# Kernel optimization log

Measured on AMD Instinct MI355X. Metric: run time of the kernel, lower is better.

## Reference

```python
import jax, jax.numpy as jnp
import numpy as np

B, T, C, H = 2, 4096, 1024, 16
HD = C // H  # head dim = 64


def setup_inputs() -> dict:
    key = jax.random.key(0)
    ks = jax.random.split(key, 5)
    s = 1.0 / np.sqrt(C)
    return {
        "x": jax.random.normal(ks[0], (B, T, C), jnp.float32),
        # stored as (in, out) so forward is x @ w + b (equiv to torch Linear with W^T)
        "w_attn": jax.random.normal(ks[1], (C, 3 * C), jnp.float32) * s,
        "b_attn": jax.random.normal(ks[2], (3 * C,), jnp.float32) * 0.02,
        "w_proj": jax.random.normal(ks[3], (C, C), jnp.float32) * s,
        "b_proj": jax.random.normal(ks[4], (C,), jnp.float32) * 0.02,
    }


def reference(x, w_attn, b_attn, w_proj, b_proj):
    # qkv projection: (B,T,3C) -> split into q,k,v
    qkv = x @ w_attn + b_attn
    q, k, v = jnp.split(qkv, 3, axis=-1)
    # (B,T,C) -> (B,H,T,HD)
    def to_heads(t):
        return t.reshape(B, T, H, HD).transpose(0, 2, 1, 3)
    q, k, v = to_heads(q), to_heads(k), to_heads(v)
    # naive attention: explicit (B,H,T,T) scores, causal mask, softmax
    att = jnp.einsum("bhqd,bhkd->bhqk", q, k) * (1.0 / np.sqrt(HD))
    causal = jnp.tril(jnp.ones((T, T), bool))  # (T,T)
    att = jnp.where(causal[None, None], att, -jnp.inf)
    att = jax.nn.softmax(att, axis=-1)
    y = jnp.einsum("bhqk,bhkd->bhqd", att, v)  # (B,H,T,HD)
    y = y.transpose(0, 2, 1, 3).reshape(B, T, C)
    y = y @ w_proj + b_proj
    return (y, (k, v))
```

## Files before the change

kernel.cpp:

```cpp
#include <hip/hip_runtime.h>
#include <hip/hip_bf16.h>

typedef unsigned short u16;
typedef __attribute__((ext_vector_type(8))) short short8;
typedef __attribute__((ext_vector_type(4))) short s16x4;
typedef __attribute__((ext_vector_type(4))) float f32x4;

#define T_SEQ  4096
#define HEADS  16
#define HDIM   64
#define CDIM   1024
#define MDIM   8192
#define HSZ    (T_SEQ * HDIM)
#define SEC    8388608
#define QSCALE 0.1803368801111244f

__device__ __forceinline__ u16 f2bf(float f) {
    __hip_bfloat16 h = __float2bfloat16(f);
    u16 u; __builtin_memcpy(&u, &h, 2);
    return u;
}

__global__ __launch_bounds__(256) void cast_k(const float* __restrict__ in,
                                              u16* __restrict__ out, int n4) {
    const int i = blockIdx.x * 256 + threadIdx.x;
    if (i < n4) {
        f32x4 v = ((const f32x4*)in)[i];
        s16x4 o;
        #pragma unroll
        for (int j = 0; j < 4; ++j) o[j] = (short)f2bf(v[j]);
        ((s16x4*)out)[i] = o;
    }
}

template <int IN_F32>
__global__ __launch_bounds__(256) void transpose_k(const void* __restrict__ in_,
                                                   u16* __restrict__ out,
                                                   int R, int C) {
    __shared__ u16 tile[32][33];
    const size_t zoff = (size_t)blockIdx.z * R * C;
    const int c0 = blockIdx.x * 32, r0 = blockIdx.y * 32;
    const int tx = threadIdx.x, ty = threadIdx.y;
    #pragma unroll
    for (int i = ty; i < 32; i += 8) {
        const size_t idx = zoff + (size_t)(r0 + i) * C + c0 + tx;
        tile[i][tx] = IN_F32 ? f2bf(((const float*)in_)[idx])
                             : ((const u16*)in_)[idx];
    }
    __syncthreads();
    #pragma unroll
    for (int i = ty; i < 32; i += 8)
        out[zoff + (size_t)(c0 + i) * R + r0 + tx] = tile[tx][i];
}

template <int MODE>
__global__ __launch_bounds__(256) void gemm_k(const u16* __restrict__ A,
                                              const u16* __restrict__ Bt,
                                              const float* __restrict__ bias,
                                              float* __restrict__ outp,
                                              u16* __restrict__ qws,
                                              u16* __restrict__ kbf, int K) {
    __shared__ unsigned char sA[16384];
    __shared__ unsigned char sB[16384];
    const int tid  = threadIdx.x;
    const int lane = tid & 63;
    const int w = tid >> 6, wr = w >> 1, wc = w & 1;
    const int m0 = blockIdx.y * 128, n0 = blockIdx.x * 128;
    const int fr = lane & 15, fg = lane >> 4;

    f32x4 acc[4][4] = {};

    const int srow  = tid >> 1;
    const int scolb = (tid & 1) * 64;
    const u16* ga = A  + (size_t)(m0 + srow) * K + (tid & 1) * 32;
    const u16* gb = Bt + (size_t)(n0 + srow) * K + (tid & 1) * 32;
    unsigned char* wAr = sA + srow * 128;
    unsigned char* wBr = sB + srow * 128;
    const int swz  = (srow & 7) << 4;
    const int rswz = (fr & 7) << 4;

    const int nk = K >> 6;
    for (int kt = 0; kt < nk; ++kt) {
        short8 va0 = *(const short8*)(ga + 0);
        short8 va1 = *(const short8*)(ga + 8);
        short8 va2 = *(const short8*)(ga + 16);
        short8 va3 = *(const short8*)(ga + 24);
        short8 vb0 = *(const short8*)(gb + 0);
        short8 vb1 = *(const short8*)(gb + 8);
        short8 vb2 = *(const short8*)(gb + 16);
        short8 vb3 = *(const short8*)(gb + 24);
        ga += 64; gb += 64;
        __syncthreads();
        *(short8*)(wAr + ((scolb +  0) ^ swz)) = va0;
        *(short8*)(wAr + ((scolb + 16) ^ swz)) = va1;
        *(short8*)(wAr + ((scolb + 32) ^ swz)) = va2;
        *(short8*)(wAr + ((scolb + 48) ^ swz)) = va3;
        *(short8*)(wBr + ((scolb +  0) ^ swz)) = vb0;
        *(short8*)(wBr + ((scolb + 16) ^ swz)) = vb1;
        *(short8*)(wBr + ((scolb + 32) ^ swz)) = vb2;
        *(short8*)(wBr + ((scolb + 48) ^ swz)) = vb3;
        __syncthreads();
        #pragma unroll
        for (int kk = 0; kk < 2; ++kk) {
            short8 af[4], bf[4];
            #pragma unroll
            for (int m = 0; m < 4; ++m)
                af[m] = *(const short8*)(sA + (wr*64 + m*16 + fr) * 128 +
                                         ((kk*64 + fg*16) ^ rswz));
            #pragma unroll
            for (int n = 0; n < 4; ++n)
                bf[n] = *(const short8*)(sB + (wc*64 + n*16 + fr) * 128 +
                                         ((kk*64 + fg*16) ^ rswz));
            #pragma unroll
            for (int m = 0; m < 4; ++m)
                #pragma unroll
                for (int n = 0; n < 4; ++n)
                    acc[m][n] = __builtin_amdgcn_mfma_f32_16x16x32_bf16(
                        af[m], bf[n], acc[m][n], 0, 0, 0);
        }
    }

    #pragma unroll
    for (int n = 0; n < 4; ++n) {
        const int gn = n0 + wc*64 + n*16 + fr;
        const float bn = bias[gn];
        if (MODE == 0) {
            const int s = gn >> 10;
            const int c = gn & 1023;
            const int h = c >> 6, d = c & 63;
            if (s == 0) {
                #pragma unroll
                for (int m = 0; m < 4; ++m)
                    #pragma unroll
                    for (int r = 0; r < 4; ++r) {
                        const int gm = m0 + wr*64 + m*16 + fg*4 + r;
                        const int b = gm >> 12, t = gm & 4095;
                        qws[(size_t)((b << 4) + h) * HSZ + (size_t)t * HDIM + d] =
                            f2bf((acc[m][n][r] + bn) * QSCALE);
                    }
            } else {
                float* fdst = outp + (size_t)s * SEC;
                #pragma unroll
                for (int m = 0; m < 4; ++m)
                    #pragma unroll
                    for (int r = 0; r < 4; ++r) {
                        const int gm = m0 + wr*64 + m*16 + fg*4 + r;
                        const int b = gm >> 12, t = gm & 4095;
                        const size_t hidx =
                            (size_t)((b << 4) + h) * HSZ + (size_t)t * HDIM + d;
                        const float v = acc[m][n][r] + bn;
                        fdst[hidx] = v;
                        if (s == 1 && kbf) kbf[hidx] = f2bf(v);
                    }
            }
        } else {
            #pragma unroll
            for (int m = 0; m < 4; ++m)
                #pragma unroll
                for (int r = 0; r < 4; ++r) {
                    const int gm = m0 + wr*64 + m*16 + fg*4 + r;
                    outp[(size_t)gm * CDIM + gn] = acc[m][n][r] + bn;
                }
        }
    }
}

template <int KBF>
__global__ __launch_bounds__(256) void attn_k(const u16* __restrict__ q,
                                              const float* __restrict__ kf32,
                                              const u16* __restrict__ kb16,
                                              const u16* __restrict__ vt,
                                              u16* __restrict__ att) {
    __shared__ unsigned char sK[4096];
    __shared__ unsigned char sV[4096];
    __shared__ unsigned char sP[4096];
    const int wg  = blockIdx.x;
    const int xcd = wg & 7;
    const int i   = wg >> 3;
    const int bh  = xcd * 4 + (i >> 5);
    const int pair = i & 31;
    const int tid = threadIdx.x, lane = tid & 63, w = tid >> 6;
    const int fr = lane & 15, fg = lane >> 4;
    const size_t hbase = (size_t)bh * HSZ;

    const int krow = tid >> 3, kcolb = (tid & 7) * 16;
    const int swzK = (krow & 7) << 4;
    const int vrow = tid >> 2, vcolb = (tid & 3) * 16;
    const int swzV = (vrow & 3) << 4;
    const int rswzK = (fr & 7) << 4;
    const int rswzV = (fr & 3) << 4;
    const int rswzP = (((fr & 3) ^ ((fr >> 2) & 3)) << 4);

    const float* gkf = kf32 ? kf32 + hbase + (size_t)krow * 64 + (tid & 7) * 8 : nullptr;
    const u16*   gkb = kb16 ? kb16 + hbase + (size_t)krow * 64 + (tid & 7) * 8 : nullptr;
    const u16*   gv  = vt + hbase + (size_t)vrow * T_SEQ + (tid & 3) * 8;
    const int b = bh >> 4, h = bh & 15;

    #pragma unroll
    for (int ph = 0; ph < 2; ++ph) {
        const int qblk = ph ? 63 - pair : pair;
        const int q0 = qblk * 64 + w * 16;

        const short8 qf0 = *(const short8*)(q + hbase + (size_t)(q0 + fr) * 64 + fg * 8);
        const short8 qf1 = *(const short8*)(q + hbase + (size_t)(q0 + fr) * 64 + 32 + fg * 8);

        f32x4 o[4] = {};
        float srow[4] = {0.f, 0.f, 0.f, 0.f};

        const int nkt = 2 * (qblk + 1);
        for (int kt = 0; kt < nkt; ++kt) {
            short8 kv;
            if (KBF) {
                kv = *(const short8*)(gkb + (size_t)kt * 2048);
            } else {
                f32x4 ka = *(const f32x4*)(gkf + (size_t)kt * 2048);
                f32x4 kb = *(const f32x4*)(gkf + (size_t)kt * 2048 + 4);
                #pragma unroll
                for (int j = 0; j < 4; ++j) {
                    kv[j]     = (short)f2bf(ka[j]);
                    kv[4 + j] = (short)f2bf(kb[j]);
                }
            }
            short8 vv = *(const short8*)(gv + kt * 32);
            __syncthreads();
            *(short8*)(sK + krow * 128 + (kcolb ^ swzK)) = kv;
            *(short8*)(sV + vrow * 64  + (vcolb ^ swzV)) = vv;
            __syncthreads();

            f32x4 sc[2];
            #pragma unroll
            for (int kh = 0; kh < 2; ++kh) {
                short8 kf0 = *(const short8*)(sK + (kh*16 + fr) * 128 +
                                              ((fg*16) ^ rswzK));
                short8 kf1 = *(const short8*)(sK + (kh*16 + fr) * 128 +
                                              ((64 + fg*16) ^ rswzK));
                f32x4 z = {0.f, 0.f, 0.f, 0.f};
                z = __builtin_amdgcn_mfma_f32_16x16x32_bf16(qf0, kf0, z, 0, 0, 0);
                z = __builtin_amdgcn_mfma_f32_16x16x32_bf16(qf1, kf1, z, 0, 0, 0);
                sc[kh] = z;
            }

            const int kb2 = kt * 32;
            const bool full = (kb2 + 31 <= q0);
            #pragma unroll
            for (int r = 0; r < 4; ++r) {
                const int qg = q0 + fg * 4 + r;
                float s0 = sc[0][r], s1 = sc[1][r];
                if (!full) {
                    s0 = (kb2 + fr      <= qg) ? s0 : -1e30f;
                    s1 = (kb2 + 16 + fr <= qg) ? s1 : -1e30f;
                }
                const float p0 = exp2f(s0);
                const float p1 = exp2f(s1);
                srow[r] += p0 + p1;
                const int prow = fg * 4 + r;
                const int sw = ((r ^ fg) & 3) << 4;
                *(u16*)(sP + w*1024 + prow*64 + ((fr*2)      ^ sw)) = f2bf(p0);
                *(u16*)(sP + w*1024 + prow*64 + ((32 + fr*2) ^ sw)) = f2bf(p1);
            }

            asm volatile("s_waitcnt lgkmcnt(0)" ::: "memory");
            __builtin_amdgcn_sched_barrier(0);

            short8 pf = *(const short8*)(sP + w*1024 + fr*64 + ((fg*16) ^ rswzP));
            #pragma unroll
            for (int db = 0; db < 4; ++db) {
                short8 vf = *(const short8*)(sV + (db*16 + fr) * 64 +
                                             ((fg*16) ^ rswzV));
                o[db] = __builtin_amdgcn_mfma_f32_16x16x32_bf16(pf, vf, o[db], 0, 0, 0);
            }
        }

        #pragma unroll
        for (int r = 0; r < 4; ++r) {
            float rs = srow[r];
            rs += __shfl_xor(rs, 1, 64);
            rs += __shfl_xor(rs, 2, 64);
            rs += __shfl_xor(rs, 4, 64);
            rs += __shfl_xor(rs, 8, 64);
            const float inv = 1.f / rs;
            #pragma unroll
            for (int db = 0; db < 4; ++db) {
                const int t = q0 + fg * 4 + r;
                att[(size_t)(b * T_SEQ + t) * CDIM + h * 64 + db * 16 + fr] =
                    f2bf(o[db][r] * inv);
            }
        }
    }
}

extern "C" void kernel_launch(void* const* d_in, const int* in_sizes, int n_in,
                              void* d_out, int out_size, void* d_ws, size_t ws_size,
                              hipStream_t stream) {
    (void)out_size;
    const float *x = nullptr, *w_attn = nullptr, *b_attn = nullptr,
                *w_proj = nullptr, *b_proj = nullptr;
    for (int i = 0; i < n_in; ++i) {
        switch (in_sizes[i]) {
            case 8388608: x      = (const float*)d_in[i]; break;
            case 3145728: w_attn = (const float*)d_in[i]; break;
            case 3072:    b_attn = (const float*)d_in[i]; break;
            case 1048576: w_proj = (const float*)d_in[i]; break;
            case 1024:    b_proj = (const float*)d_in[i]; break;
        }
    }
    if (!x || !w_attn || !b_attn || !w_proj || !b_proj) return;

    float* out = (float*)d_out;
    unsigned char* ws = (unsigned char*)d_ws;
    const bool big = ws_size >= (64ull << 20);

    u16* q_ws = (u16*)(ws);
    u16* wTp  = (u16*)(ws);
    u16* x_bf = (u16*)(ws + 16777216);
    u16* vT   = (u16*)(ws + 16777216);
    u16* wTa  = (u16*)(ws + 33554432);
    u16* attb = (u16*)(ws + 33554432);
    u16* k_bf = big ? (u16*)(ws + 50331648) : nullptr;

    cast_k<<<8192, 256, 0, stream>>>(x, x_bf, 2097152);
    transpose_k<1><<<dim3(96, 32, 1), dim3(32, 8), 0, stream>>>(w_attn, wTa, 1024, 3072);
    gemm_k<0><<<dim3(24, 64), 256, 0, stream>>>(x_bf, wTa, b_attn, out, q_ws, k_bf, 1024);
    transpose_k<1><<<dim3(2, 128, 32), dim3(32, 8), 0, stream>>>(out + 2 * (size_t)SEC, vT, 4096, 64);
    if (big)
        attn_k<1><<<1024, 256, 0, stream>>>(q_ws, nullptr, k_bf, vT, attb);
    else
        attn_k<0><<<1024, 256, 0, stream>>>(q_ws, out + SEC, nullptr, vT, attb);
    transpose_k<1><<<dim3(32, 32, 1), dim3(32, 8), 0, stream>>>(w_proj, wTp, 1024, 1024);
    gemm_k<1><<<dim3(8, 64), 256, 0, stream>>>(attb, wTp, b_proj, out, nullptr, nullptr, 1024);
}
```

Measured before the change: 293.5 us.

## Compute transposed scores so P stays in registers, dropping LDS round-trip

Swaps the MFMA operand order so each lane holds score columns for one query row, which lets the softmax probabilities be packed straight into the PV MFMA A-operand in registers. This removes the per-tile P staging buffer in shared memory, its waitcnt and scheduling barrier. To match the key order that register layout implies, the V transpose kernel permutes its output columns within each 32-key block. Row sums are now reduced across lane groups and the inverse is shuffled back to output rows. This depends on the permutation exactly matching the MFMA register layout.

```diff
diff --git a/kernel.cpp b/kernel.cpp
--- a/kernel.cpp
+++ b/kernel.cpp
@@ -33,7 +33,7 @@
     }
 }
 
-template <int IN_F32>
+template <int IN_F32, int PERM5>
 __global__ __launch_bounds__(256) void transpose_k(const void* __restrict__ in_,
                                                    u16* __restrict__ out,
                                                    int R, int C) {
@@ -48,9 +48,10 @@
                              : ((const u16*)in_)[idx];
     }
     __syncthreads();
+    const int txo = PERM5 ? (((tx & 12) << 1) + (tx & 3) + ((tx & 16) >> 2)) : tx;
     #pragma unroll
     for (int i = ty; i < 32; i += 8)
-        out[zoff + (size_t)(c0 + i) * R + r0 + tx] = tile[tx][i];
+        out[zoff + (size_t)(c0 + i) * R + r0 + txo] = tile[tx][i];
 }
 
 template <int MODE>
@@ -173,7 +174,6 @@
                                               u16* __restrict__ att) {
     __shared__ unsigned char sK[4096];
     __shared__ unsigned char sV[4096];
-    __shared__ unsigned char sP[4096];
     const int wg  = blockIdx.x;
     const int xcd = wg & 7;
     const int i   = wg >> 3;
@@ -189,7 +189,6 @@
     const int swzV = (vrow & 3) << 4;
     const int rswzK = (fr & 7) << 4;
     const int rswzV = (fr & 3) << 4;
-    const int rswzP = (((fr & 3) ^ ((fr >> 2) & 3)) << 4);
 
     const float* gkf = kf32 ? kf32 + hbase + (size_t)krow * 64 + (tid & 7) * 8 : nullptr;
     const u16*   gkb = kb16 ? kb16 + hbase + (size_t)krow * 64 + (tid & 7) * 8 : nullptr;
@@ -205,7 +204,7 @@
         const short8 qf1 = *(const short8*)(q + hbase + (size_t)(q0 + fr) * 64 + 32 + fg * 8);
 
         f32x4 o[4] = {};
-        float srow[4] = {0.f, 0.f, 0.f, 0.f};
+        float ssum = 0.f;
 
         const int nkt = 2 * (qblk + 1);
         for (int kt = 0; kt < nkt; ++kt) {
@@ -227,42 +226,47 @@
             *(short8*)(sV + vrow * 64  + (vcolb ^ swzV)) = vv;
             __syncthreads();
 
-            f32x4 sc[2];
+            f32x4 z[2];
             #pragma unroll
             for (int kh = 0; kh < 2; ++kh) {
-                short8 kf0 = *(const short8*)(sK + (kh*16 + fr) * 128 +
+                short8 kfa = *(const short8*)(sK + (kh*16 + fr) * 128 +
                                               ((fg*16) ^ rswzK));
-                short8 kf1 = *(const short8*)(sK + (kh*16 + fr) * 128 +
+                short8 kfb = *(const short8*)(sK + (kh*16 + fr) * 128 +
                                               ((64 + fg*16) ^ rswzK));
-                f32x4 z = {0.f, 0.f, 0.f, 0.f};
-                z = __builtin_amdgcn_mfma_f32_16x16x32_bf16(qf0, kf0, z, 0, 0, 0);
-                z = __builtin_amdgcn_mfma_f32_16x16x32_bf16(qf1, kf1, z, 0, 0, 0);
-                sc[kh] = z;
+                f32x4 zz = {0.f, 0.f, 0.f, 0.f};
+                zz = __builtin_amdgcn_mfma_f32_16x16x32_bf16(kfa, qf0, zz, 0, 0, 0);
+                zz = __builtin_amdgcn_mfma_f32_16x16x32_bf16(kfb, qf1, zz, 0, 0, 0);
+                z[kh] = zz;
             }
 
             const int kb2 = kt * 32;
             const bool full = (kb2 + 31 <= q0);
+            const int kq = kb2 + fg * 4;
+            const int qg = q0 + fr;
+            float p[8];
             #pragma unroll
             for (int r = 0; r < 4; ++r) {
-                const int qg = q0 + fg * 4 + r;
-                float s0 = sc[0][r], s1 = sc[1][r];
+                float s0 = z[0][r], s1 = z[1][r];
                 if (!full) {
-                    s0 = (kb2 + fr      <= qg) ? s0 : -1e30f;
-                    s1 = (kb2 + 16 + fr <= qg) ? s1 : -1e30f;
+                    s0 = (kq + r      <= qg) ? s0 : -1e30f;
+                    s1 = (kq + 16 + r <= qg) ? s1 : -1e30f;
                 }
-                const float p0 = exp2f(s0);
-                const float p1 = exp2f(s1);
-                srow[r] += p0 + p1;
-                const int prow = fg * 4 + r;
-                const int sw = ((r ^ fg) & 3) << 4;
-                *(u16*)(sP + w*1024 + prow*64 + ((fr*2)      ^ sw)) = f2bf(p0);
-                *(u16*)(sP + w*1024 + prow*64 + ((32 + fr*2) ^ sw)) = f2bf(p1);
-            }
-
-            asm volatile("s_waitcnt lgkmcnt(0)" ::: "memory");
-            __builtin_amdgcn_sched_barrier(0);
-
-            short8 pf = *(const short8*)(sP + w*1024 + fr*64 + ((fg*16) ^ rswzP));
+                p[r]     = exp2f(s0);
+                p[4 + r] = exp2f(s1);
+            }
+            ssum += p[0] + p[1] + p[2] + p[3] + p[4] + p[5] + p[6] + p[7];
+
+            unsigned int pw0, pw1, pw2, pw3;
+            asm("v_cvt_pk_bf16_f32 %0, %1, %2" : "=v"(pw0) : "v"(p[0]), "v"(p[1]));
+            asm("v_cvt_pk_bf16_f32 %0, %1, %2" : "=v"(pw1) : "v"(p[2]), "v"(p[3]));
+            asm("v_cvt_pk_bf16_f32 %0, %1, %2" : "=v"(pw2) : "v"(p[4]), "v"(p[5]));
+            asm("v_cvt_pk_bf16_f32 %0, %1, %2" : "=v"(pw3) : "v"(p[6]), "v"(p[7]));
+            short8 pf;
+            {
+                unsigned int tmp[4] = {pw0, pw1, pw2, pw3};
+                __builtin_memcpy(&pf, tmp, 16);
+            }
+
             #pragma unroll
             for (int db = 0; db < 4; ++db) {
                 short8 vf = *(const short8*)(sV + (db*16 + fr) * 64 +
@@ -271,19 +275,18 @@
             }
         }
 
+        float rs = ssum;
+        rs += __shfl_xor(rs, 16, 64);
+        rs += __shfl_xor(rs, 32, 64);
+        const float inv = 1.f / rs;
         #pragma unroll
         for (int r = 0; r < 4; ++r) {
-            float rs = srow[r];
-            rs += __shfl_xor(rs, 1, 64);
-            rs += __shfl_xor(rs, 2, 64);
-            rs += __shfl_xor(rs, 4, 64);
-            rs += __shfl_xor(rs, 8, 64);
-            const float inv = 1.f / rs;
+            const float invq = __shfl(inv, (fg << 4) + (fg << 2) + r, 64);
+            const int t = q0 + fg * 4 + r;
             #pragma unroll
             for (int db = 0; db < 4; ++db) {
-                const int t = q0 + fg * 4 + r;
                 att[(size_t)(b * T_SEQ + t) * CDIM + h * 64 + db * 16 + fr] =
-                    f2bf(o[db][r] * inv);
+                    f2bf(o[db][r] * invq);
             }
         }
     }
@@ -319,13 +322,13 @@
     u16* k_bf = big ? (u16*)(ws + 50331648) : nullptr;
 
     cast_k<<<8192, 256, 0, stream>>>(x, x_bf, 2097152);
-    transpose_k<1><<<dim3(96, 32, 1), dim3(32, 8), 0, stream>>>(w_attn, wTa, 1024, 3072);
+    transpose_k<1, 0><<<dim3(96, 32, 1), dim3(32, 8), 0, stream>>>(w_attn, wTa, 1024, 3072);
     gemm_k<0><<<dim3(24, 64), 256, 0, stream>>>(x_bf, wTa, b_attn, out, q_ws, k_bf, 1024);
-    transpose_k<1><<<dim3(2, 128, 32), dim3(32, 8), 0, stream>>>(out + 2 * (size_t)SEC, vT, 4096, 64);
+    transpose_k<1, 1><<<dim3(2, 128, 32), dim3(32, 8), 0, stream>>>(out + 2 * (size_t)SEC, vT, 4096, 64);
     if (big)
         attn_k<1><<<1024, 256, 0, stream>>>(q_ws, nullptr, k_bf, vT, attb);
     else
         attn_k<0><<<1024, 256, 0, stream>>>(q_ws, out + SEC, nullptr, vT, attb);
-    transpose_k<1><<<dim3(32, 32, 1), dim3(32, 8), 0, stream>>>(w_proj, wTp, 1024, 1024);
+    transpose_k<1, 0><<<dim3(32, 32, 1), dim3(32, 8), 0, stream>>>(w_proj, wTp, 1024, 1024);
     gemm_k<1><<<dim3(8, 64), 256, 0, stream>>>(attb, wTp, b_proj, out, nullptr, nullptr, 1024);
 }
```

New measurement: 275.6 us. 1.06x faster.
